# Performance work log

Measured on AMD Instinct MI355X. Metric: run time of the kernel, lower is better.

Reference implementation:

```python
import jax, jax.numpy as jnp
import numpy as np

B, S, D = 8, 4096, 1024       # batch, seq_len, d_model
WIN = 257                     # window_size (odd): keys [i-128, i+128]
HALF = WIN // 2               # 128
BL = 256                      # block length for banded attention (BL >= HALF, S % BL == 0)


def setup_inputs() -> dict:
    key = jax.random.key(0)
    ks = jax.random.split(key, 7)
    s = 0.02
    return {
        "x":  jax.random.normal(ks[0], (B, S, D), jnp.float32),
        "Wq": jax.random.normal(ks[1], (D, D), jnp.float32) * s,
        "bq": jnp.zeros((D,), jnp.float32),
        "Wk": jax.random.normal(ks[2], (D, D), jnp.float32) * s,
        "bk": jnp.zeros((D,), jnp.float32),
        "Wv": jax.random.normal(ks[3], (D, D), jnp.float32) * s,
        "bv": jnp.zeros((D,), jnp.float32),
    }


def _blockify(t, nb):
    # t: [B, S, D] -> [B, nb, 3*BL, D]; for block b, keys from blocks b-1, b, b+1 (zero-padded at edges)
    b, s, d = t.shape
    tp = jnp.pad(t, ((0, 0), (BL, BL), (0, 0)))
    tb = tp.reshape(b, nb + 2, BL, d)
    return jnp.concatenate([tb[:, :-2], tb[:, 1:-1], tb[:, 2:]], axis=2)


def _local_attention(q, k, v):
    # Faithful vectorized form of the per-token sliding-window loop:
    # for each i: keys/values from [max(0, i-HALF), min(S, i+HALF+1)), scaled-dot softmax.
    b, s, d = q.shape
    nb = s // BL
    qb = q.reshape(b, nb, BL, d)
    kb = _blockify(k, nb)                          # [B, nb, 3BL, D]
    vb = _blockify(v, nb)
    scale = 1.0 / np.sqrt(d).astype(np.float32)    # d_model ** 0.5 (scaled_dot)
    scores = jnp.einsum('bnqd,bnkd->bnqk', qb, kb) * scale  # [B, nb, BL, 3BL]

    blk = jnp.arange(nb)[:, None, None]
    r = jnp.arange(BL)[None, :, None]
    c = jnp.arange(3 * BL)[None, None, :]
    i = blk * BL + r                               # global query position
    j = (blk - 1) * BL + c                         # global key position
    rel = j - i
    valid = (rel >= -HALF) & (rel <= HALF) & (j >= 0) & (j < s)  # [nb, BL, 3BL]

    scores = jnp.where(valid[None], scores, -jnp.inf)
    weights = jax.nn.softmax(scores, axis=-1)
    out = jnp.einsum('bnqk,bnkd->bnqd', weights, vb)
    return out.reshape(b, s, d)


def reference(x, Wq, bq, Wk, bk, Wv, bv) -> jnp.ndarray:
    q = x @ Wq + bq
    k = x @ Wk + bk
    v = x @ Wv + bv
    return _local_attention(q, k, v)
```

## Files before the change

kernel.cpp:

```cpp
#include <hip/hip_runtime.h>
#include <hip/hip_fp16.h>
#include <cstdint>


#define DEV __device__ __forceinline__

typedef _Float16 f16x8 __attribute__((ext_vector_type(8)));
typedef _Float16 f16x4 __attribute__((ext_vector_type(4)));
typedef float    f32x4 __attribute__((ext_vector_type(4)));

DEV _Float16 f2h(float f) { return (_Float16)f; }

DEV void gl16(const void* g, void* l) {
  __builtin_amdgcn_global_load_lds(
      (const __attribute__((address_space(1))) void*)(uintptr_t)g,
      (__attribute__((address_space(3))) void*)(uintptr_t)l, 16, 0, 0);
}

#define MFMA16(a, b, c) __builtin_amdgcn_mfma_f32_16x16x32_f16((a), (b), (c), 0, 0, 0)

__global__ __launch_bounds__(256) void k_cvt_x(const float* __restrict__ x,
                                               _Float16* __restrict__ xh) {
  size_t i = ((size_t)blockIdx.x * 256 + threadIdx.x) * 8;
  float4 f0 = *(const float4*)(x + i);
  float4 f1 = *(const float4*)(x + i + 4);
  f16x8 o;
  o[0] = f2h(f0.x); o[1] = f2h(f0.y); o[2] = f2h(f0.z); o[3] = f2h(f0.w);
  o[4] = f2h(f1.x); o[5] = f2h(f1.y); o[6] = f2h(f1.z); o[7] = f2h(f1.w);
  *(f16x8*)(xh + i) = o;
}

__global__ __launch_bounds__(256) void k_cvt_w(const float* __restrict__ Wq,
                                               const float* __restrict__ Wk,
                                               const float* __restrict__ Wv,
                                               _Float16* __restrict__ wt) {
  __shared__ float tile[64][65];
  const int z = blockIdx.z;
  const int n0 = blockIdx.x * 64, k0 = blockIdx.y * 64;
  const float* W = (z == 0) ? Wq : (z == 1) ? Wk : Wv;
  const int tid = threadIdx.x;
  const int r0 = tid >> 4;
  const int c4 = (tid & 15) * 4;
#pragma unroll
  for (int rr = 0; rr < 4; ++rr) {
    int r = r0 + rr * 16;
    float4 v = *(const float4*)(W + (size_t)(k0 + r) * 1024 + n0 + c4);
    tile[r][c4 + 0] = v.x; tile[r][c4 + 1] = v.y;
    tile[r][c4 + 2] = v.z; tile[r][c4 + 3] = v.w;
  }
  __syncthreads();
  _Float16* out = wt + (size_t)z * 1048576;
#pragma unroll
  for (int rr = 0; rr < 4; ++rr) {
    int n = r0 + rr * 16;
    f16x4 o;
#pragma unroll
    for (int jj = 0; jj < 4; ++jj) o[jj] = f2h(tile[c4 + jj][n]);
    *(f16x4*)(out + (size_t)(n0 + n) * 1024 + k0 + c4) = o;
  }
}

__global__ __launch_bounds__(512, 2) void k_gemm_qkv(
    const _Float16* __restrict__ xh, const _Float16* __restrict__ wt,
    const float* __restrict__ bq, const float* __restrict__ bk,
    const float* __restrict__ bv, _Float16* __restrict__ qh,
    _Float16* __restrict__ kh, _Float16* __restrict__ v8) {
  __shared__ _Float16 L[65536];

  const int bid = blockIdx.x;
  const int wg = (bid & 7) * 192 + (bid >> 3);
  const int mt = wg / 12, nt = wg % 12;
  const int gm0 = mt * 256;
  const int gn0 = nt * 256;

  const int tid = threadIdx.x;
  const int w = tid >> 6, l = tid & 63;
  const int ln = l & 15, quad = l >> 4;
  const int wm = w >> 2, wn = w & 3;
  const int lr = l >> 3;
  const int kc = ((l & 7) ^ lr) * 8;
  const int swz = ln & 7;

  auto stageA = [&](int it, int h) {
    const _Float16* src =
        xh + (size_t)(gm0 + h * 128 + w * 8 + lr) * 1024 + it * 64 + kc;
    _Float16* dst = L + (it & 1) * 32768 + (h * 128 + w * 8) * 64;
    gl16(src, dst);
    gl16(src + 64 * 1024, dst + 64 * 64);
  };
  auto stageB = [&](int it, int h) {
    const _Float16* src =
        wt + (size_t)(gn0 + h * 128 + w * 8 + lr) * 1024 + it * 64 + kc;
    _Float16* dst = L + (it & 1) * 32768 + 16384 + (h * 128 + w * 8) * 64;
    gl16(src, dst);
    gl16(src + 64 * 1024, dst + 64 * 64);
  };

#define RD(base, r, ko) \
  (*(const f16x8*)((base) + (size_t)(r) * 64 + (((ko) ^ swz) * 8)))

  f32x4 acc[8][4] = {};
  f16x8 aA[2][4], bb0[2][2], bb1[2][2];

  stageA(0, 0); stageA(0, 1); stageB(0, 0); stageB(0, 1);
  stageB(1, 0); stageB(1, 1);
  asm volatile("s_waitcnt vmcnt(4)" ::: "memory");
  __builtin_amdgcn_s_barrier();

#pragma unroll 2
  for (int t = 0; t < 16; ++t) {
    const _Float16* Ab = L + (t & 1) * 32768;
    const _Float16* Bb = Ab + 16384;
    const int rA = wm * 128 + ln;
    const int rB = wn * 64 + ln;

#pragma unroll
    for (int i = 0; i < 4; ++i) {
      aA[0][i] = RD(Ab, rA + i * 16, quad);
      aA[1][i] = RD(Ab, rA + i * 16, quad + 4);
    }
#pragma unroll
    for (int j = 0; j < 2; ++j) {
      bb0[0][j] = RD(Bb, rB + j * 16, quad);
      bb0[1][j] = RD(Bb, rB + j * 16, quad + 4);
    }
    if (t + 1 < 16) stageA(t + 1, 0);
    __builtin_amdgcn_s_barrier();
    asm volatile("s_waitcnt lgkmcnt(0)" ::: "memory");
    __builtin_amdgcn_sched_barrier(0);
    __builtin_amdgcn_s_setprio(1);
#pragma unroll
    for (int s = 0; s < 2; ++s)
#pragma unroll
      for (int i = 0; i < 4; ++i)
#pragma unroll
        for (int j = 0; j < 2; ++j)
          acc[i][j] = MFMA16(aA[s][i], bb0[s][j], acc[i][j]);
    __builtin_amdgcn_s_setprio(0);
    __builtin_amdgcn_s_barrier();

#pragma unroll
    for (int j = 0; j < 2; ++j) {
      bb1[0][j] = RD(Bb, rB + 32 + j * 16, quad);
      bb1[1][j] = RD(Bb, rB + 32 + j * 16, quad + 4);
    }
    if (t + 1 < 16) stageA(t + 1, 1);
    __builtin_amdgcn_s_barrier();
    asm volatile("s_waitcnt lgkmcnt(0)" ::: "memory");
    __builtin_amdgcn_sched_barrier(0);
    __builtin_amdgcn_s_setprio(1);
#pragma unroll
    for (int s = 0; s < 2; ++s)
#pragma unroll
      for (int i = 0; i < 4; ++i)
#pragma unroll
        for (int j = 0; j < 2; ++j)
          acc[i][2 + j] = MFMA16(aA[s][i], bb1[s][j], acc[i][2 + j]);
    __builtin_amdgcn_s_setprio(0);
    __builtin_amdgcn_s_barrier();

#pragma unroll
    for (int i = 0; i < 4; ++i) {
      aA[0][i] = RD(Ab, rA + 64 + i * 16, quad);
      aA[1][i] = RD(Ab, rA + 64 + i * 16, quad + 4);
    }
    if (t + 2 < 16) stageB(t + 2, 0);
    __builtin_amdgcn_s_barrier();
    asm volatile("s_waitcnt lgkmcnt(0)" ::: "memory");
    __builtin_amdgcn_sched_barrier(0);
    __builtin_amdgcn_s_setprio(1);
#pragma unroll
    for (int s = 0; s < 2; ++s)
#pragma unroll
      for (int i = 0; i < 4; ++i)
#pragma unroll
        for (int j = 0; j < 2; ++j)
          acc[4 + i][2 + j] = MFMA16(aA[s][i], bb1[s][j], acc[4 + i][2 + j]);
    __builtin_amdgcn_s_setprio(0);
    __builtin_amdgcn_s_barrier();

    if (t + 2 < 16) stageB(t + 2, 1);
    __builtin_amdgcn_s_setprio(1);
#pragma unroll
    for (int s = 0; s < 2; ++s)
#pragma unroll
      for (int i = 0; i < 4; ++i)
#pragma unroll
        for (int j = 0; j < 2; ++j)
          acc[4 + i][j] = MFMA16(aA[s][i], bb0[s][j], acc[4 + i][j]);
    __builtin_amdgcn_s_setprio(0);
    if (t + 2 < 16)
      asm volatile("s_waitcnt vmcnt(4)" ::: "memory");
    else
      asm volatile("s_waitcnt vmcnt(0)" ::: "memory");
    __builtin_amdgcn_s_barrier();
  }
#undef RD

  const int z2 = gn0 >> 10;
  const int colz = (gn0 & 1023) + wn * 64;
  const int row0 = gm0 + wm * 128;
  if (z2 != 2) {
    const float* bias = z2 ? bk : bq;
    _Float16* outp = z2 ? kh : qh;
#pragma unroll
    for (int j = 0; j < 4; ++j) {
      float bb = bias[colz + j * 16 + ln];
#pragma unroll
      for (int i = 0; i < 8; ++i) {
        int row = row0 + i * 16 + quad * 4;
        size_t base = (size_t)row * 1024 + colz + j * 16 + ln;
#pragma unroll
        for (int r = 0; r < 4; ++r)
          outp[base + (size_t)r * 1024] = f2h(acc[i][j][r] + bb);
      }
    }
  } else {
#pragma unroll
    for (int j = 0; j < 4; ++j) {
      float bb = bv[colz + j * 16 + ln];
#pragma unroll
      for (int i = 0; i < 8; ++i) {
        int rr = row0 + i * 16 + quad * 4;
        int col = colz + j * 16 + ln;
        f16x4 o;
#pragma unroll
        for (int r = 0; r < 4; ++r) o[r] = f2h(acc[i][j][r] + bb);
        *(f16x4*)(v8 + (size_t)(rr >> 3) * 8192 + (size_t)col * 8 + (rr & 7)) = o;
      }
    }
  }
}

__global__ __launch_bounds__(512, 2) void k_attn(const _Float16* __restrict__ qh,
                                                 const _Float16* __restrict__ kh,
                                                 const _Float16* __restrict__ v8,
                                                 float* __restrict__ out) {
  __shared__ _Float16 smem[73728];
  const int t = blockIdx.x, b = blockIdx.y;
  const int i0 = t * 128, k0 = i0 - 128;
  const int tid = threadIdx.x, w = tid >> 6, l = tid & 63;
  const int ln = l & 15, quad = l >> 4;
  const int wm2 = w >> 2, wn4 = w & 3;
  const _Float16* qrow = qh + (size_t)b * 4096 * 1024;
  const _Float16* krow = kh + (size_t)b * 4096 * 1024;
  const _Float16* vb = v8 + (size_t)b * 4194304;
  const int kc = ((l & 7) ^ (l >> 3)) * 8;
  const int swz = ln & 7;

  auto stage = [&](int it) {
    int buf = it & 1;
#pragma unroll
    for (int c = 0; c < 2; ++c) {
      int cid = w * 2 + c;
      int rl = cid * 8 + (l >> 3);
      gl16(qrow + (size_t)(i0 + rl) * 1024 + it * 64 + kc,
           &smem[buf * 8192 + cid * 512]);
    }
#pragma unroll
    for (int c = 0; c < 6; ++c) {
      int cid = w * 6 + c;
      int rl = cid * 8 + (l >> 3);
      int gr = min(max(k0 + rl, 0), 4095);
      gl16(krow + (size_t)gr * 1024 + it * 64 + kc,
           &smem[16384 + buf * 24576 + cid * 512]);
    }
  };

  f32x4 s[4][6] = {};

  stage(0);
  asm volatile("s_waitcnt vmcnt(0)" ::: "memory");
  __builtin_amdgcn_s_barrier();

  for (int it = 0; it < 16; ++it) {
    int buf = it & 1;
    if (it + 1 < 16) stage(it + 1);
    f16x8 af[2][4], bf[2][6];
#pragma unroll
    for (int i = 0; i < 4; ++i) {
      int r = wm2 * 64 + i * 16 + ln;
      af[0][i] = *(const f16x8*)(&smem[buf * 8192 + r * 64 + ((quad ^ swz) * 8)]);
      af[1][i] = *(const f16x8*)(&smem[buf * 8192 + r * 64 + (((quad + 4) ^ swz) * 8)]);
    }
#pragma unroll
    for (int j = 0; j < 6; ++j) {
      int r = wn4 * 96 + j * 16 + ln;
      bf[0][j] = *(const f16x8*)(&smem[16384 + buf * 24576 + r * 64 + ((quad ^ swz) * 8)]);
      bf[1][j] = *(const f16x8*)(&smem[16384 + buf * 24576 + r * 64 + (((quad + 4) ^ swz) * 8)]);
    }
    asm volatile("s_waitcnt lgkmcnt(0)" ::: "memory");
    __builtin_amdgcn_sched_barrier(0);
    __builtin_amdgcn_s_setprio(1);
#pragma unroll
    for (int ss = 0; ss < 2; ++ss)
#pragma unroll
      for (int i = 0; i < 4; ++i)
#pragma unroll
        for (int j = 0; j < 6; ++j)
          s[i][j] = MFMA16(af[ss][i], bf[ss][j], s[i][j]);
    __builtin_amdgcn_s_setprio(0);
    asm volatile("s_waitcnt vmcnt(0)" ::: "memory");
    __builtin_amdgcn_s_barrier();
  }

  float* redM = (float*)(&smem[65536]);
  float* redS = redM + 512;
  const float scale = 0.03125f;
  float mrow[4][4];
#pragma unroll
  for (int i = 0; i < 4; ++i)
#pragma unroll
    for (int r = 0; r < 4; ++r) mrow[i][r] = -1e30f;
#pragma unroll
  for (int j = 0; j < 6; ++j) {
    int jc = k0 + wn4 * 96 + j * 16 + ln;
    bool cval = (jc >= 0) && (jc < 4096);
#pragma unroll
    for (int i = 0; i < 4; ++i)
#pragma unroll
      for (int r = 0; r < 4; ++r) {
        int iq = i0 + wm2 * 64 + i * 16 + quad * 4 + r;
        int rel = jc - iq;
        bool val = cval && (rel >= -128) && (rel <= 128);
        float sc = val ? s[i][j][r] * scale : -1e30f;
        s[i][j][r] = sc;
        mrow[i][r] = fmaxf(mrow[i][r], sc);
      }
  }
#pragma unroll
  for (int i = 0; i < 4; ++i)
#pragma unroll
    for (int r = 0; r < 4; ++r)
#pragma unroll
      for (int m = 1; m < 16; m <<= 1)
        mrow[i][r] = fmaxf(mrow[i][r], __shfl_xor(mrow[i][r], m));
  if (ln == 0) {
#pragma unroll
    for (int i = 0; i < 4; ++i)
#pragma unroll
      for (int r = 0; r < 4; ++r)
        redM[wn4 * 128 + wm2 * 64 + i * 16 + quad * 4 + r] = mrow[i][r];
  }
  __syncthreads();
  float mf[4][4];
#pragma unroll
  for (int i = 0; i < 4; ++i)
#pragma unroll
    for (int r = 0; r < 4; ++r) {
      int row = wm2 * 64 + i * 16 + quad * 4 + r;
      mf[i][r] = fmaxf(fmaxf(redM[row], redM[128 + row]),
                       fmaxf(redM[256 + row], redM[384 + row]));
    }
  float srow[4][4] = {};
#pragma unroll
  for (int j = 0; j < 6; ++j)
#pragma unroll
    for (int i = 0; i < 4; ++i)
#pragma unroll
      for (int r = 0; r < 4; ++r) {
        float e = __builtin_exp2f((s[i][j][r] - mf[i][r]) * 1.44269504f);
        s[i][j][r] = e;
        srow[i][r] += e;
      }
#pragma unroll
  for (int i = 0; i < 4; ++i)
#pragma unroll
    for (int r = 0; r < 4; ++r)
#pragma unroll
      for (int m = 1; m < 16; m <<= 1) srow[i][r] += __shfl_xor(srow[i][r], m);
  if (ln == 0) {
#pragma unroll
    for (int i = 0; i < 4; ++i)
#pragma unroll
      for (int r = 0; r < 4; ++r)
        redS[wn4 * 128 + wm2 * 64 + i * 16 + quad * 4 + r] = srow[i][r];
  }
  __syncthreads();
  float inv[4][4];
#pragma unroll
  for (int i = 0; i < 4; ++i)
#pragma unroll
    for (int r = 0; r < 4; ++r) {
      int row = wm2 * 64 + i * 16 + quad * 4 + r;
      inv[i][r] = 1.0f / (redS[row] + redS[128 + row] + redS[256 + row] + redS[384 + row]);
    }
#pragma unroll
  for (int j = 0; j < 6; ++j) {
    int col = wn4 * 96 + j * 16 + ln;
    int oct = col >> 3, e = col & 7;
#pragma unroll
    for (int i = 0; i < 4; ++i)
#pragma unroll
      for (int r = 0; r < 4; ++r) {
        int row = wm2 * 64 + i * 16 + quad * 4 + r;
        smem[row * 384 + ((oct ^ (row & 7)) << 3) + e] = f2h(s[i][j][r] * inv[i][r]);
      }
  }
  __syncthreads();

  const int wq = w >> 1, wn2 = w & 1;
  const int g0 = (t * 128 - 128) >> 3;
  _Float16* lV = &smem[49152];

  auto stageV = [&](int c) {
    int buf = c & 1;
    int n0 = c * 32;
#pragma unroll
    for (int cc = 0; cc < 3; ++cc) {
      int ob = w * 6 + cc * 2;
      int oct = ob + (l >> 5);
      int g = min(max(g0 + oct, 0), 511);
      gl16(vb + (size_t)g * 8192 + (size_t)(n0 + (l & 31)) * 8,
           &lV[buf * 12288 + ob * 256]);
    }
  };

  stageV(0);
  stageV(1);
  asm volatile("s_waitcnt vmcnt(3)" ::: "memory");
  __builtin_amdgcn_s_barrier();

  for (int c = 0; c < 32; ++c) {
    int buf = c & 1;
    if (c >= 1 && c + 1 < 32) stageV(c + 1);
    f32x4 acc[2] = {};
#pragma unroll
    for (int ks = 0; ks < 12; ++ks) {
      int o = ks * 4 + quad;
      int rA0 = wq * 32 + ln;
      int rA1 = rA0 + 16;
      f16x8 a0 = *(const f16x8*)(&smem[rA0 * 384 + ((o ^ (rA0 & 7)) << 3)]);
      f16x8 a1 = *(const f16x8*)(&smem[rA1 * 384 + ((o ^ (rA1 & 7)) << 3)]);
      f16x8 bv = *(const f16x8*)(&lV[buf * 12288 + (o * 32 + wn2 * 16 + ln) * 8]);
      acc[0] = MFMA16(a0, bv, acc[0]);
      acc[1] = MFMA16(a1, bv, acc[1]);
    }
    int col = c * 32 + wn2 * 16 + ln;
#pragma unroll
    for (int i = 0; i < 2; ++i) {
      int row = t * 128 + wq * 32 + i * 16 + quad * 4;
      size_t base = ((size_t)b * 4096 + row) * 1024 + col;
#pragma unroll
      for (int r = 0; r < 4; ++r) out[base + (size_t)r * 1024] = acc[i][r];
    }
    if (c + 1 < 32) {
      asm volatile("s_waitcnt vmcnt(8)" ::: "memory");
      __builtin_amdgcn_s_barrier();
    }
  }
}

extern "C" void kernel_launch(void* const* d_in, const int* in_sizes, int n_in,
                              void* d_out, int out_size, void* d_ws, size_t ws_size,
                              hipStream_t stream) {
  const float* x  = (const float*)d_in[0];
  const float* Wq = (const float*)d_in[1];
  const float* bq = (const float*)d_in[2];
  const float* Wk = (const float*)d_in[3];
  const float* bk = (const float*)d_in[4];
  const float* Wv = (const float*)d_in[5];
  const float* bv = (const float*)d_in[6];
  float* out = (float*)d_out;

  _Float16* ws = (_Float16*)d_ws;
  _Float16* xh = ws;
  _Float16* wt = ws + 33554432;
  _Float16* qh = ws + 36700160;
  _Float16* kh = ws + 70254592;
  _Float16* v8 = ws + 103809024;

  k_cvt_x<<<16384, 256, 0, stream>>>(x, xh);
  k_cvt_w<<<dim3(16, 16, 3), 256, 0, stream>>>(Wq, Wk, Wv, wt);
  k_gemm_qkv<<<dim3(1536), 512, 0, stream>>>(xh, wt, bq, bk, bv, qh, kh, v8);
  k_attn<<<dim3(32, 8), 512, 0, stream>>>(qh, kh, v8, out);
}
```

Before: 524.0 us.

## Split Q/K staging into deeper pipeline and hoist P fragments into registers

The QK^T loop now stages K two iterations ahead and Q one iteration ahead. K loads are issued mid-iteration, between two halves of the MFMA work, and the loop waits on a partial vmcnt instead of draining all loads each iteration. This is meant to hide global-to-LDS latency behind compute. In the PV loop, the probability fragments are loaded from LDS into registers once rather than on every one of the 32 column chunks. That cuts repeated LDS reads but adds 24 f16x8 registers per thread, which could raise pressure under launch_bounds(512,2). An extra barrier per iteration is added to guard Q buffer reuse.

```diff
diff --git a/kernel.cpp b/kernel.cpp
--- a/kernel.cpp
+++ b/kernel.cpp
@@ -248,7 +248,7 @@
   const int kc = ((l & 7) ^ (l >> 3)) * 8;
   const int swz = ln & 7;
 
-  auto stage = [&](int it) {
+  auto stageQ = [&](int it) {
     int buf = it & 1;
 #pragma unroll
     for (int c = 0; c < 2; ++c) {
@@ -257,6 +257,9 @@
       gl16(qrow + (size_t)(i0 + rl) * 1024 + it * 64 + kc,
            &smem[buf * 8192 + cid * 512]);
     }
+  };
+  auto stageK = [&](int it) {
+    int buf = it & 1;
 #pragma unroll
     for (int c = 0; c < 6; ++c) {
       int cid = w * 6 + c;
@@ -269,13 +272,14 @@
 
   f32x4 s[4][6] = {};
 
-  stage(0);
-  asm volatile("s_waitcnt vmcnt(0)" ::: "memory");
+  stageK(0);
+  stageQ(0);
+  stageK(1);
+  asm volatile("s_waitcnt vmcnt(6)" ::: "memory");
   __builtin_amdgcn_s_barrier();
 
   for (int it = 0; it < 16; ++it) {
     int buf = it & 1;
-    if (it + 1 < 16) stage(it + 1);
     f16x8 af[2][4], bf[2][6];
 #pragma unroll
     for (int i = 0; i < 4; ++i) {
@@ -289,18 +293,29 @@
       bf[0][j] = *(const f16x8*)(&smem[16384 + buf * 24576 + r * 64 + ((quad ^ swz) * 8)]);
       bf[1][j] = *(const f16x8*)(&smem[16384 + buf * 24576 + r * 64 + (((quad + 4) ^ swz) * 8)]);
     }
+    if (it + 1 < 16) stageQ(it + 1);
+    __builtin_amdgcn_s_barrier();
     asm volatile("s_waitcnt lgkmcnt(0)" ::: "memory");
     __builtin_amdgcn_sched_barrier(0);
     __builtin_amdgcn_s_setprio(1);
 #pragma unroll
-    for (int ss = 0; ss < 2; ++ss)
-#pragma unroll
-      for (int i = 0; i < 4; ++i)
-#pragma unroll
-        for (int j = 0; j < 6; ++j)
-          s[i][j] = MFMA16(af[ss][i], bf[ss][j], s[i][j]);
+    for (int i = 0; i < 4; ++i)
+#pragma unroll
+      for (int j = 0; j < 6; ++j)
+        s[i][j] = MFMA16(af[0][i], bf[0][j], s[i][j]);
     __builtin_amdgcn_s_setprio(0);
-    asm volatile("s_waitcnt vmcnt(0)" ::: "memory");
+    if (it + 2 < 16) stageK(it + 2);
+    __builtin_amdgcn_s_setprio(1);
+#pragma unroll
+    for (int i = 0; i < 4; ++i)
+#pragma unroll
+      for (int j = 0; j < 6; ++j)
+        s[i][j] = MFMA16(af[1][i], bf[1][j], s[i][j]);
+    __builtin_amdgcn_s_setprio(0);
+    if (it + 2 < 16)
+      asm volatile("s_waitcnt vmcnt(6)" ::: "memory");
+    else
+      asm volatile("s_waitcnt vmcnt(0)" ::: "memory");
     __builtin_amdgcn_s_barrier();
   }
 
@@ -418,6 +433,19 @@
 
   stageV(0);
   stageV(1);
+
+  f16x8 pa[2][12];
+  {
+    const int rA0 = wq * 32 + ln;
+    const int rA1 = rA0 + 16;
+#pragma unroll
+    for (int ks = 0; ks < 12; ++ks) {
+      int o = ks * 4 + quad;
+      pa[0][ks] = *(const f16x8*)(&smem[rA0 * 384 + ((o ^ (rA0 & 7)) << 3)]);
+      pa[1][ks] = *(const f16x8*)(&smem[rA1 * 384 + ((o ^ (rA1 & 7)) << 3)]);
+    }
+  }
+
   asm volatile("s_waitcnt vmcnt(3)" ::: "memory");
   __builtin_amdgcn_s_barrier();
 
@@ -428,13 +456,9 @@
 #pragma unroll
     for (int ks = 0; ks < 12; ++ks) {
       int o = ks * 4 + quad;
-      int rA0 = wq * 32 + ln;
-      int rA1 = rA0 + 16;
-      f16x8 a0 = *(const f16x8*)(&smem[rA0 * 384 + ((o ^ (rA0 & 7)) << 3)]);
-      f16x8 a1 = *(const f16x8*)(&smem[rA1 * 384 + ((o ^ (rA1 & 7)) << 3)]);
       f16x8 bv = *(const f16x8*)(&lV[buf * 12288 + (o * 32 + wn2 * 16 + ln) * 8]);
-      acc[0] = MFMA16(a0, bv, acc[0]);
-      acc[1] = MFMA16(a1, bv, acc[1]);
+      acc[0] = MFMA16(pa[0][ks], bv, acc[0]);
+      acc[1] = MFMA16(pa[1][ks], bv, acc[1]);
     }
     int col = c * 32 + wn2 * 16 + ln;
 #pragma unroll
```

After: 536.5 us. +2.4%, slower.
